# Performance work log

Measured on AMD Instinct MI355X. Metric: run time of the kernel, lower is better.

## Reference

```python
import jax, jax.numpy as jnp
import numpy as np

B, L, DIM = 2, 4096, 512
HEADS, KS = 8, 33
HEAD_DIM = DIM // HEADS
SCALE = HEAD_DIM ** -0.5


def setup_inputs() -> dict:
    key = jax.random.key(0)
    ks = jax.random.split(key, 5)
    s = 0.02
    return {
        "x": jax.random.normal(ks[0], (B, L, DIM), dtype=jnp.float32),
        "w_qkv": jax.random.normal(ks[1], (3 * DIM, DIM), dtype=jnp.float32) * s,
        "b_qkv": jax.random.normal(ks[2], (3 * DIM,), dtype=jnp.float32) * s,
        "w_proj": jax.random.normal(ks[3], (DIM, DIM), dtype=jnp.float32) * s,
        "b_proj": jax.random.normal(ks[4], (DIM,), dtype=jnp.float32) * s,
    }


def _na1d(q, k, v):
    # q,k,v: [B, L, H, d]. Each query i attends to KS tokens whose window
    # start is clamp(i - KS//2, 0, L-KS) (NATTEN boundary-clamped neighborhood).
    starts = jnp.clip(jnp.arange(L) - KS // 2, 0, L - KS)          # [L]
    idx = starts[:, None] + jnp.arange(KS)[None, :]                # [L, KS]
    k_g = k[:, idx]                                                # [B, L, KS, H, d]
    v_g = v[:, idx]                                                # [B, L, KS, H, d]
    scores = jnp.einsum("blhd,blkhd->bhlk", q * SCALE, k_g)        # [B, H, L, KS]
    attn = jax.nn.softmax(scores, axis=-1)
    out = jnp.einsum("bhlk,blkhd->blhd", attn, v_g)                # [B, L, H, d]
    return out


def reference(x, w_qkv, b_qkv, w_proj, b_proj):
    qkv = x @ w_qkv.T + b_qkv                                      # [B, L, 3*DIM]
    qkv = qkv.reshape(B, L, 3, HEADS, HEAD_DIM)
    q, k, v = qkv[:, :, 0], qkv[:, :, 1], qkv[:, :, 2]
    out = _na1d(q, k, v).reshape(B, L, DIM)
    return out @ w_proj.T + b_proj
```

## Files before the change

### kernel.cpp

```cpp
#include <hip/hip_runtime.h>
#include <hip/hip_bf16.h>

#define B_ 2
#define L_ 4096
#define DIM_ 512
#define HEADS_ 8
#define HDIM_ 64
#define KS_ 33

typedef __bf16 bf16;
typedef __bf16 bf16x4 __attribute__((ext_vector_type(4)));
typedef __bf16 bf16x8 __attribute__((ext_vector_type(8)));
typedef float f32x4 __attribute__((ext_vector_type(4)));

typedef __attribute__((address_space(3))) void lds_void;
typedef __attribute__((address_space(1))) const void glb_void;

__device__ __forceinline__ void async_cp16(const bf16* g, bf16* l)
{
    __builtin_amdgcn_global_load_lds((glb_void*)g, (lds_void*)l, 16, 0, 0);
}

__global__ __launch_bounds__(256)
void cvt_all(const float* __restrict__ x,  const float* __restrict__ wq,
             const float* __restrict__ bq, const float* __restrict__ wp,
             const float* __restrict__ bp,
             bf16* __restrict__ xb,  bf16* __restrict__ wqb,
             bf16* __restrict__ bqb, bf16* __restrict__ wpb,
             bf16* __restrict__ bpb)
{
    const int blk = blockIdx.x;
    const float* src; bf16* dst; int n, base;
    if (blk < 2048)       { src = x;  dst = xb;  n = 4194304; base = blk; }
    else if (blk < 2432)  { src = wq; dst = wqb; n = 786432;  base = blk - 2048; }
    else if (blk < 2560)  { src = wp; dst = wpb; n = 262144;  base = blk - 2432; }
    else if (blk == 2560) { src = bq; dst = bqb; n = 1536;    base = 0; }
    else                  { src = bp; dst = bpb; n = 512;     base = 0; }
    int i = base * 2048 + threadIdx.x * 8;
    if (i + 8 <= n) {
        float4 a = *(const float4*)(src + i);
        float4 b = *(const float4*)(src + i + 4);
        bf16x8 o;
        o[0] = (bf16)a.x; o[1] = (bf16)a.y; o[2] = (bf16)a.z; o[3] = (bf16)a.w;
        o[4] = (bf16)b.x; o[5] = (bf16)b.y; o[6] = (bf16)b.z; o[7] = (bf16)b.w;
        *(bf16x8*)(dst + i) = o;
    }
}

template <typename OutT>
__global__ __launch_bounds__(256)
void gemm_nt_bias(const bf16* __restrict__ A, const bf16* __restrict__ W,
                  const bf16* __restrict__ bias, OutT* __restrict__ C,
                  int M, int N, int K)
{
    __shared__ bf16 As[128][64];
    __shared__ bf16 Bs[128][64];

    const int tid  = threadIdx.x;
    const int wave = tid >> 6;
    const int lane = tid & 63;
    const int wm   = (wave >> 1) * 64;
    const int wn   = (wave & 1) * 64;
    const int l16  = lane & 15;
    const int quad = lane >> 4;

    const int row0 = blockIdx.x * 128;
    const int col0 = blockIdx.y * 128;

    f32x4 acc[4][4] = {};

    for (int k0 = 0; k0 < K; k0 += 64) {
        #pragma unroll
        for (int it = 0; it < 4; ++it) {
            int f   = it * 256 + tid;
            int r   = f >> 3;
            int c8l = (f & 7) ^ (r & 7);
            async_cp16(&A[(size_t)(row0 + r) * K + k0 + c8l * 8], &As[r][(f & 7) * 8]);
            async_cp16(&W[(size_t)(col0 + r) * K + k0 + c8l * 8], &Bs[r][(f & 7) * 8]);
        }
        __syncthreads();

        #pragma unroll
        for (int ks = 0; ks < 2; ++ks) {
            bf16x8 af[4], bfr[4];
            #pragma unroll
            for (int i = 0; i < 4; ++i) {
                int ra = wm + i * 16 + l16;
                int rb = wn + i * 16 + l16;
                af[i]  = *(const bf16x8*)(&As[ra][((ks * 4 + quad) ^ (ra & 7)) * 8]);
                bfr[i] = *(const bf16x8*)(&Bs[rb][((ks * 4 + quad) ^ (rb & 7)) * 8]);
            }
            #pragma unroll
            for (int mi = 0; mi < 4; ++mi)
                #pragma unroll
                for (int ni = 0; ni < 4; ++ni)
                    acc[mi][ni] = __builtin_amdgcn_mfma_f32_16x16x32_bf16(
                        af[mi], bfr[ni], acc[mi][ni], 0, 0, 0);
        }
        __syncthreads();
    }

    #pragma unroll
    for (int ni = 0; ni < 4; ++ni) {
        int n = col0 + wn + ni * 16 + l16;
        float bv = (float)bias[n];
        #pragma unroll
        for (int mi = 0; mi < 4; ++mi) {
            int mrow = row0 + wm + mi * 16 + quad * 4;
            #pragma unroll
            for (int r = 0; r < 4; ++r)
                C[(size_t)(mrow + r) * N + n] = (OutT)(acc[mi][ni][r] + bv);
        }
    }
}

__global__ __launch_bounds__(256)
void na1d_attn_mfma(const bf16* __restrict__ qkv, bf16* __restrict__ att)
{
    __shared__ bf16 Plds[4][16][72];

    const int wave = threadIdx.x >> 6;
    const int lane = threadIdx.x & 63;
    const int l16  = lane & 15;
    const int quad = lane >> 4;

    const int wid = blockIdx.x * 4 + wave;
    const int qg  = wid & 255;
    const int bh  = wid >> 8;
    const int h   = bh & 7;
    const int b   = bh >> 3;
    const int q0  = qg * 16;

    int k_base = q0 - 16;
    if (k_base < 0) k_base = 0;
    if (k_base > L_ - KS_) k_base = L_ - KS_;

    const size_t rs = 3 * DIM_;

    const bf16* qptr = qkv + (size_t)(b * L_ + q0 + l16) * rs + h * HDIM_ + quad * 8;
    bf16x8 qf0 = *(const bf16x8*)(qptr);
    bf16x8 qf1 = *(const bf16x8*)(qptr + 32);

    const bf16* kcol = qkv + (size_t)(b * L_ + k_base) * rs + DIM_ + h * HDIM_;
    f32x4 s[3] = {};
    #pragma unroll
    for (int t = 0; t < 3; ++t) {
        const bf16* kptr = kcol + (size_t)(t * 16 + l16) * rs + quad * 8;
        bf16x8 kf0 = *(const bf16x8*)(kptr);
        bf16x8 kf1 = *(const bf16x8*)(kptr + 32);
        s[t] = __builtin_amdgcn_mfma_f32_16x16x32_bf16(qf0, kf0, s[t], 0, 0, 0);
        s[t] = __builtin_amdgcn_mfma_f32_16x16x32_bf16(qf1, kf1, s[t], 0, 0, 0);
    }

    int offr[4];
    #pragma unroll
    for (int r = 0; r < 4; ++r) {
        int lq = q0 + quad * 4 + r;
        int st = lq - KS_ / 2;
        if (st < 0) st = 0;
        if (st > L_ - KS_) st = L_ - KS_;
        offr[r] = st - k_base;
    }
    float sv[3][4];
    #pragma unroll
    for (int t = 0; t < 3; ++t) {
        int j = t * 16 + l16;
        #pragma unroll
        for (int r = 0; r < 4; ++r) {
            float x = s[t][r] * 0.125f;
            sv[t][r] = (j >= offr[r] && j <= offr[r] + 32) ? x : -1e30f;
        }
    }

    float mr[4], sum[4];
    #pragma unroll
    for (int r = 0; r < 4; ++r)
        mr[r] = fmaxf(fmaxf(sv[0][r], sv[1][r]), sv[2][r]);
    #pragma unroll
    for (int o = 1; o < 16; o <<= 1)
        #pragma unroll
        for (int r = 0; r < 4; ++r)
            mr[r] = fmaxf(mr[r], __shfl_xor(mr[r], o, 64));
    #pragma unroll
    for (int t = 0; t < 3; ++t)
        #pragma unroll
        for (int r = 0; r < 4; ++r)
            sv[t][r] = __expf(sv[t][r] - mr[r]);
    #pragma unroll
    for (int r = 0; r < 4; ++r)
        sum[r] = sv[0][r] + sv[1][r] + sv[2][r];
    #pragma unroll
    for (int o = 1; o < 16; o <<= 1)
        #pragma unroll
        for (int r = 0; r < 4; ++r)
            sum[r] += __shfl_xor(sum[r], o, 64);
    #pragma unroll
    for (int r = 0; r < 4; ++r) {
        float inv = 1.0f / sum[r];
        #pragma unroll
        for (int t = 0; t < 3; ++t) sv[t][r] *= inv;
    }

    bf16* P = &Plds[wave][0][0];
    {
        int rr = lane >> 2;
        int c0 = 48 + (lane & 3) * 4;
        *(bf16x4*)(&P[rr * 72 + c0]) = (bf16x4){(bf16)0.f, (bf16)0.f, (bf16)0.f, (bf16)0.f};
    }
    #pragma unroll
    for (int t = 0; t < 3; ++t)
        #pragma unroll
        for (int r = 0; r < 4; ++r)
            P[(quad * 4 + r) * 72 + t * 16 + l16] = (bf16)sv[t][r];
    __syncthreads();

    bf16x8 pf0 = *(const bf16x8*)(&P[l16 * 72 + quad * 8]);
    bf16x8 pf1 = *(const bf16x8*)(&P[l16 * 72 + 32 + quad * 8]);

    const bf16* vcol = qkv + (size_t)(b * L_ + k_base) * rs + 2 * DIM_ + h * HDIM_;
    f32x4 o[4] = {};
    #pragma unroll
    for (int t = 0; t < 4; ++t) {
        bf16x8 vf0, vf1;
        #pragma unroll
        for (int j = 0; j < 8; ++j) {
            vf0[j] = vcol[(size_t)(quad * 8 + j) * rs + t * 16 + l16];
            vf1[j] = vcol[(size_t)(32 + quad * 8 + j) * rs + t * 16 + l16];
        }
        o[t] = __builtin_amdgcn_mfma_f32_16x16x32_bf16(pf0, vf0, o[t], 0, 0, 0);
        o[t] = __builtin_amdgcn_mfma_f32_16x16x32_bf16(pf1, vf1, o[t], 0, 0, 0);
    }

    bf16* orow = att + (size_t)(b * L_ + q0) * DIM_ + h * HDIM_;
    #pragma unroll
    for (int t = 0; t < 4; ++t)
        #pragma unroll
        for (int r = 0; r < 4; ++r)
            orow[(size_t)(quad * 4 + r) * DIM_ + t * 16 + l16] = (bf16)o[t][r];
}

extern "C" void kernel_launch(void* const* d_in, const int* in_sizes, int n_in,
                              void* d_out, int out_size, void* d_ws, size_t ws_size,
                              hipStream_t stream) {
    const int n_x  = B_ * L_ * DIM_;
    const int n_wq = 3 * DIM_ * DIM_;
    const int n_bq = 3 * DIM_;
    const int n_wp = DIM_ * DIM_;
    const int n_bp = DIM_;

    char* ws = (char*)d_ws;
    bf16* xb  = (bf16*)ws;
    bf16* wqb = xb  + n_x;
    bf16* bqb = wqb + n_wq;
    bf16* wpb = bqb + n_bq;
    bf16* bpb = wpb + n_wp;
    bf16* qkv = bpb + n_bp;
    bf16* att = qkv + (size_t)8192 * 1536;

    float* out = (float*)d_out;
    const int M = B_ * L_;

    cvt_all<<<2562, 256, 0, stream>>>(
        (const float*)d_in[0], (const float*)d_in[1], (const float*)d_in[2],
        (const float*)d_in[3], (const float*)d_in[4],
        xb, wqb, bqb, wpb, bpb);

    gemm_nt_bias<bf16><<<dim3(M / 128, (3 * DIM_) / 128), 256, 0, stream>>>(
        xb, wqb, bqb, qkv, M, 3 * DIM_, DIM_);

    na1d_attn_mfma<<<dim3((B_ * HEADS_ * L_) / 64), 256, 0, stream>>>(qkv, att);

    gemm_nt_bias<float><<<dim3(M / 128, DIM_ / 128), 256, 0, stream>>>(
        att, wpb, bpb, out, M, DIM_, DIM_);
}
```

Baseline: 125.7 us.

## Stage shared K/V window in LDS per block and remap blocks across XCDs

Each block of four waves (64 queries) now loads one 96-row K/V window into LDS, so neighbouring query tiles share it instead of each wave reading K and V from global memory with strided per-element loads. K is copied asynchronously into LDS with an XOR swizzle, and V is stored with row padding so that later column reads avoid bank conflicts. The block index is decoded so that adjacent sequence chunks are spread across XCDs. This adds LDS traffic and a block-wide barrier before compute, and padded rows are clamped at the sequence edges.

```diff
diff --git a/kernel.cpp b/kernel.cpp
--- a/kernel.cpp
+++ b/kernel.cpp
@@ -117,45 +117,81 @@
 __global__ __launch_bounds__(256)
 void na1d_attn_mfma(const bf16* __restrict__ qkv, bf16* __restrict__ att)
 {
+    __shared__ bf16 Klds[96 * 64];
+    __shared__ bf16 Vlds[96 * 66];
     __shared__ bf16 Plds[4][16][72];
 
-    const int wave = threadIdx.x >> 6;
-    const int lane = threadIdx.x & 63;
+    const int tid  = threadIdx.x;
+    const int wave = tid >> 6;
+    const int lane = tid & 63;
     const int l16  = lane & 15;
     const int quad = lane >> 4;
 
-    const int wid = blockIdx.x * 4 + wave;
-    const int qg  = wid & 255;
-    const int bh  = wid >> 8;
-    const int h   = bh & 7;
-    const int b   = bh >> 3;
-    const int q0  = qg * 16;
-
-    int k_base = q0 - 16;
-    if (k_base < 0) k_base = 0;
-    if (k_base > L_ - KS_) k_base = L_ - KS_;
+    const int xcd  = blockIdx.x & 7;
+    const int s    = blockIdx.x >> 3;
+    const int jj   = s & 3;
+    const int half = (s >> 2) & 1;
+    const int h    = (s >> 3) & 7;
+    const int b    = s >> 6;
+    const int p    = jj * 8 + xcd;
+    const int Q0   = p * 128 + half * 64;
 
     const size_t rs = 3 * DIM_;
-
-    const bf16* qptr = qkv + (size_t)(b * L_ + q0 + l16) * rs + h * HDIM_ + quad * 8;
+    const size_t rowbase = (size_t)b * L_;
+
+    #pragma unroll
+    for (int i = 0; i < 3; ++i) {
+        int ck = i * 256 + tid;
+        int r  = ck >> 3;
+        int pc = ck & 7;
+        int lc = pc ^ (r & 7);
+        int g  = Q0 - 16 + r;
+        g = g < 0 ? 0 : (g > L_ - 1 ? L_ - 1 : g);
+        async_cp16(qkv + (rowbase + g) * rs + DIM_ + h * HDIM_ + lc * 8,
+                   Klds + (size_t)ck * 8);
+    }
+    {
+        unsigned int* V32 = (unsigned int*)Vlds;
+        #pragma unroll
+        for (int i = 0; i < 3; ++i) {
+            int cv = i * 256 + tid;
+            int r  = cv >> 3;
+            int pc = cv & 7;
+            int g  = Q0 - 16 + r;
+            g = g < 0 ? 0 : (g > L_ - 1 ? L_ - 1 : g);
+            uint4 val = *(const uint4*)(qkv + (rowbase + g) * rs + 2 * DIM_ + h * HDIM_ + pc * 8);
+            int base = r * 33 + pc * 4;
+            V32[base + 0] = val.x; V32[base + 1] = val.y;
+            V32[base + 2] = val.z; V32[base + 3] = val.w;
+        }
+    }
+
+    const int q0w = Q0 + wave * 16;
+    const bf16* qptr = qkv + (rowbase + q0w + l16) * rs + h * HDIM_ + quad * 8;
     bf16x8 qf0 = *(const bf16x8*)(qptr);
     bf16x8 qf1 = *(const bf16x8*)(qptr + 32);
 
-    const bf16* kcol = qkv + (size_t)(b * L_ + k_base) * rs + DIM_ + h * HDIM_;
-    f32x4 s[3] = {};
+    int k_base = q0w - 16;
+    if (k_base > L_ - 48) k_base = L_ - 48;
+    if (k_base < 0) k_base = 0;
+    const int rel = k_base - (Q0 - 16);
+
+    __syncthreads();
+
+    f32x4 sacc[3] = {};
     #pragma unroll
     for (int t = 0; t < 3; ++t) {
-        const bf16* kptr = kcol + (size_t)(t * 16 + l16) * rs + quad * 8;
-        bf16x8 kf0 = *(const bf16x8*)(kptr);
-        bf16x8 kf1 = *(const bf16x8*)(kptr + 32);
-        s[t] = __builtin_amdgcn_mfma_f32_16x16x32_bf16(qf0, kf0, s[t], 0, 0, 0);
-        s[t] = __builtin_amdgcn_mfma_f32_16x16x32_bf16(qf1, kf1, s[t], 0, 0, 0);
+        int r = rel + t * 16 + l16;
+        bf16x8 kf0 = *(const bf16x8*)(Klds + r * 64 + ((quad ^ (r & 7)) * 8));
+        bf16x8 kf1 = *(const bf16x8*)(Klds + r * 64 + (((4 + quad) ^ (r & 7)) * 8));
+        sacc[t] = __builtin_amdgcn_mfma_f32_16x16x32_bf16(qf0, kf0, sacc[t], 0, 0, 0);
+        sacc[t] = __builtin_amdgcn_mfma_f32_16x16x32_bf16(qf1, kf1, sacc[t], 0, 0, 0);
     }
 
     int offr[4];
     #pragma unroll
     for (int r = 0; r < 4; ++r) {
-        int lq = q0 + quad * 4 + r;
+        int lq = q0w + quad * 4 + r;
         int st = lq - KS_ / 2;
         if (st < 0) st = 0;
         if (st > L_ - KS_) st = L_ - KS_;
@@ -167,8 +203,8 @@
         int j = t * 16 + l16;
         #pragma unroll
         for (int r = 0; r < 4; ++r) {
-            float x = s[t][r] * 0.125f;
-            sv[t][r] = (j >= offr[r] && j <= offr[r] + 32) ? x : -1e30f;
+            float xv = sacc[t][r] * 0.125f;
+            sv[t][r] = (j >= offr[r] && j <= offr[r] + 32) ? xv : -1e30f;
         }
     }
 
@@ -217,21 +253,20 @@
     bf16x8 pf0 = *(const bf16x8*)(&P[l16 * 72 + quad * 8]);
     bf16x8 pf1 = *(const bf16x8*)(&P[l16 * 72 + 32 + quad * 8]);
 
-    const bf16* vcol = qkv + (size_t)(b * L_ + k_base) * rs + 2 * DIM_ + h * HDIM_;
     f32x4 o[4] = {};
     #pragma unroll
     for (int t = 0; t < 4; ++t) {
         bf16x8 vf0, vf1;
         #pragma unroll
         for (int j = 0; j < 8; ++j) {
-            vf0[j] = vcol[(size_t)(quad * 8 + j) * rs + t * 16 + l16];
-            vf1[j] = vcol[(size_t)(32 + quad * 8 + j) * rs + t * 16 + l16];
+            vf0[j] = Vlds[(rel + quad * 8 + j) * 66 + t * 16 + l16];
+            vf1[j] = Vlds[(rel + 32 + quad * 8 + j) * 66 + t * 16 + l16];
         }
         o[t] = __builtin_amdgcn_mfma_f32_16x16x32_bf16(pf0, vf0, o[t], 0, 0, 0);
         o[t] = __builtin_amdgcn_mfma_f32_16x16x32_bf16(pf1, vf1, o[t], 0, 0, 0);
     }
 
-    bf16* orow = att + (size_t)(b * L_ + q0) * DIM_ + h * HDIM_;
+    bf16* orow = att + (rowbase + q0w) * DIM_ + h * HDIM_;
     #pragma unroll
     for (int t = 0; t < 4; ++t)
         #pragma unroll
```

After: 123.2 us. 2.0% less time.
